# Kernel tuning notes

Measured on AMD Instinct MI355X. Metric: run time of the kernel, lower is better.

Reference implementation:

```python
import jax, jax.numpy as jnp
import numpy as np
from jax import lax

B, N, C = 32, 1024, 768
H_RES, W_RES = 32, 32
NUM_HEADS = 8
CH = C // NUM_HEADS  # 96
SCALE = CH ** -0.5


def setup_inputs() -> dict:
    key = jax.random.key(0)
    k1, k2, k3 = jax.random.split(key, 3)
    x = jax.random.normal(k1, (B, N, C), dtype=jnp.float32)
    # trunc_normal_(std=0.02) approximated by normal * 0.02
    w_qkv = jax.random.normal(k2, (3 * C, C), dtype=jnp.float32) * 0.02
    # conv init: normal(0, sqrt(2/fan_out)), fan_out = 3*3*C/groups = 9
    w_crpe = jax.random.normal(k3, (C, 1, 3, 3), dtype=jnp.float32) * np.sqrt(2.0 / 9.0)
    b_crpe = jnp.zeros((C,), dtype=jnp.float32)
    return {"x": x, "w_qkv": w_qkv, "w_crpe": w_crpe, "b_crpe": b_crpe}


def _forward(x, w_qkv, w_crpe, b_crpe):
    b, n, c = x.shape
    h, ch = NUM_HEADS, CH
    # qkv projection: [B,N,3C] -> [3,B,h,N,Ch]
    qkv = jnp.einsum('bnc,dc->bnd', x, w_qkv)
    qkv = qkv.reshape(b, n, 3, h, ch).transpose(2, 0, 3, 1, 4)
    q, k, v = qkv[0], qkv[1], qkv[2]  # each [B,h,N,Ch]
    # softmax over token dim (dim=2 of [B,h,N,Ch])
    k_softmax = jax.nn.softmax(k, axis=2)
    # dd_trans = k_softmax^T @ v : [B,h,Ch,Ch]
    dd_trans = jnp.einsum('bhnc,bhnd->bhcd', k_softmax, v)
    factor_attn = jnp.einsum('bhnc,bhcd->bhnd', q, dd_trans)  # [B,h,N,Ch]
    # crpe: depthwise 3x3 conv on v reshaped to image layout
    v_img = v.transpose(0, 1, 3, 2).reshape(b, c, H_RES, W_RES)  # B (h Ch) H W
    conv_v = lax.conv_general_dilated(
        v_img, w_crpe, window_strides=(1, 1), padding='SAME',
        feature_group_count=c,
        dimension_numbers=('NCHW', 'OIHW', 'NCHW'))
    conv_v = conv_v + b_crpe[None, :, None, None]
    conv_v = conv_v.reshape(b, h, ch, n).transpose(0, 1, 3, 2)  # [B,h,N,Ch]
    crpe = q * conv_v
    out = SCALE * factor_attn + crpe  # [B,h,N,Ch]
    return out.transpose(0, 2, 1, 3).reshape(b, n, c)


def reference(x, w_qkv, w_crpe, b_crpe):
    return _forward(x, w_qkv, w_crpe, b_crpe)
```

## Files before the change

kernel.cpp:

```cpp
#include <hip/hip_runtime.h>
#include <stdint.h>

#define B_SZ   32
#define N_TOK  1024
#define C_DIM  768
#define HEADS  8
#define CH_DIM 96
#define GM     32768
#define GN     2304
#define GK     768
#define SCALE_F 0.10206207261596577f
#define WHICH_STRIDE 25165824u
#define BH_STRIDE    98304u

typedef __attribute__((ext_vector_type(8))) short short8;
typedef __attribute__((ext_vector_type(8))) unsigned short ushort8;
typedef __attribute__((ext_vector_type(4))) float f32x4;
typedef __attribute__((ext_vector_type(4))) int int4v;

__device__ __forceinline__ float bf2f(unsigned short u) {
  union { unsigned int i; float f; } x; x.i = ((unsigned int)u) << 16; return x.f;
}
__device__ __forceinline__ unsigned short f2bf(float f) {
  union { float f; unsigned int i; } x; x.f = f;
  unsigned int r = x.i + 0x7fffu + ((x.i >> 16) & 1u);
  return (unsigned short)(r >> 16);
}

__device__ __forceinline__ void gload_lds16(const void* g, void* l) {
  __builtin_amdgcn_global_load_lds(
      (const __attribute__((address_space(1))) unsigned int*)g,
      (__attribute__((address_space(3))) unsigned int*)l, 16, 0, 0);
}

__global__ __launch_bounds__(256) void quant_rows(
    const float* __restrict__ x, const float* __restrict__ wq,
    signed char* __restrict__ xq, signed char* __restrict__ wqo,
    float* __restrict__ inv_x, float* __restrict__ inv_w) {
  const int row = blockIdx.x * 4 + (threadIdx.x >> 6);
  const int l = threadIdx.x & 63;
  const float* src; signed char* dst; float* inv; int r;
  if (row < GM) { src = x;  dst = xq;  inv = inv_x; r = row; }
  else { r = row - GM; if (r >= GN) return; src = wq; dst = wqo; inv = inv_w; }

  const float4* s4 = (const float4*)(src + (size_t)r * 768);
  float4 v0 = s4[l], v1 = s4[l + 64], v2 = s4[l + 128];
  float m = fmaxf(fmaxf(fmaxf(fabsf(v0.x), fabsf(v0.y)), fmaxf(fabsf(v0.z), fabsf(v0.w))),
                  fmaxf(fmaxf(fabsf(v1.x), fabsf(v1.y)), fmaxf(fabsf(v1.z), fabsf(v1.w))));
  m = fmaxf(m, fmaxf(fmaxf(fabsf(v2.x), fabsf(v2.y)), fmaxf(fabsf(v2.z), fabsf(v2.w))));
#pragma unroll
  for (int off = 32; off; off >>= 1) m = fmaxf(m, __shfl_xor(m, off));
  const float sc = 127.0f / m;
  if (l == 0) inv[r] = m * (1.0f / 127.0f);

  char4* d4 = (char4*)(dst + (size_t)r * 768);
  char4 o;
  o.x = (signed char)(int)rintf(v0.x * sc); o.y = (signed char)(int)rintf(v0.y * sc);
  o.z = (signed char)(int)rintf(v0.z * sc); o.w = (signed char)(int)rintf(v0.w * sc);
  d4[l] = o;
  o.x = (signed char)(int)rintf(v1.x * sc); o.y = (signed char)(int)rintf(v1.y * sc);
  o.z = (signed char)(int)rintf(v1.z * sc); o.w = (signed char)(int)rintf(v1.w * sc);
  d4[l + 64] = o;
  o.x = (signed char)(int)rintf(v2.x * sc); o.y = (signed char)(int)rintf(v2.y * sc);
  o.z = (signed char)(int)rintf(v2.z * sc); o.w = (signed char)(int)rintf(v2.w * sc);
  d4[l + 128] = o;
}

__global__ __launch_bounds__(512, 4) void qkv_gemm_i8(
    const signed char* __restrict__ xb,
    const signed char* __restrict__ wb,
    const float* __restrict__ inv_x,
    const float* __restrict__ inv_w,
    unsigned short* __restrict__ qkv) {
  __shared__ __align__(16) char lds[3][24576];

  const int t = threadIdx.x, w = t >> 6, l = t & 63;
  const int l15 = l & 15, lhi = l >> 4;

  const int bid = blockIdx.x;
  const int swz = (bid & 7) * 288 + (bid >> 3);
  const int brow = (swz / 9) * 128;
  const int bcol = (swz % 9) * 256;
  const int wr = w >> 2, wc = w & 3;

  const int s_colb = (((l & 3) ^ ((l >> 3) & 3)) << 4);
  const char* gA0 = (const char*)xb + (size_t)brow * 768 + s_colb;
  const char* gB0 = (const char*)wb + (size_t)bcol * 768 + s_colb;

  const int rd_sw = (lhi * 16) ^ (((l15 >> 1) & 3) << 4);
  const int a_off = (wr * 64 + l15) * 64 + rd_sw;
  const int b_off = 8192 + (wc * 64 + l15) * 64 + rd_sw;

  int4v acc[4][4];
#pragma unroll
  for (int m = 0; m < 4; ++m)
#pragma unroll
    for (int n = 0; n < 4; ++n) acc[m][n] = (int4v){0, 0, 0, 0};

  auto STAGE = [&](int bi, int kt) {
    const int rowL = w * 16 + (l >> 2);
    gload_lds16(gA0 + (size_t)rowL * 768 + kt * 64,         &lds[bi][w * 1024]);
    gload_lds16(gB0 + (size_t)rowL * 768 + kt * 64,         &lds[bi][8192 + w * 1024]);
    gload_lds16(gB0 + (size_t)(rowL + 128) * 768 + kt * 64, &lds[bi][8192 + (w + 8) * 1024]);
  };

  auto COMPUTE = [&](int bi) {
    int4v af[4], bf8[4];
#pragma unroll
    for (int n = 0; n < 4; ++n)
      bf8[n] = *(const int4v*)(&lds[bi][b_off + n * 1024]);
#pragma unroll
    for (int m = 0; m < 4; ++m)
      af[m] = *(const int4v*)(&lds[bi][a_off + m * 1024]);
    __builtin_amdgcn_s_setprio(1);
#pragma unroll
    for (int m = 0; m < 4; ++m)
#pragma unroll
      for (int n = 0; n < 4; ++n)
        acc[m][n] = __builtin_amdgcn_mfma_i32_16x16x64_i8(af[m], bf8[n], acc[m][n], 0, 0, 0);
    __builtin_amdgcn_s_setprio(0);
  };

#define SB __builtin_amdgcn_sched_barrier(0)
#define BAR do { SB; __builtin_amdgcn_s_barrier(); SB; } while (0)

  STAGE(0, 0); STAGE(1, 1); STAGE(2, 2);
  SB; asm volatile("s_waitcnt vmcnt(6)" ::: "memory");
  BAR;

#pragma unroll
  for (int kt = 0; kt < 12; ++kt) {
    COMPUTE(kt % 3);
    BAR;
    if (kt < 9) {
      STAGE(kt % 3, kt + 3);
      SB; asm volatile("s_waitcnt vmcnt(6)" ::: "memory");
    } else if (kt == 9) {
      SB; asm volatile("s_waitcnt vmcnt(3)" ::: "memory");
    } else if (kt == 10) {
      SB; asm volatile("s_waitcnt vmcnt(0)" ::: "memory");
    }
    BAR;
  }

  const int bb = brow / 1024;
#pragma unroll
  for (int m = 0; m < 4; ++m) {
    const int row0 = brow + wr * 64 + m * 16 + lhi * 4;
    const int tok0 = row0 & 1023;
    float ix[4];
#pragma unroll
    for (int r = 0; r < 4; ++r) ix[r] = inv_x[row0 + r];
#pragma unroll
    for (int n = 0; n < 4; ++n) {
      const int col   = bcol + wc * 64 + n * 16 + l15;
      const float dq0 = inv_w[col];
      const int which = col / 768;
      const int hh    = (col % 768) / 96;
      const int ch    = col % 96;
      unsigned short* dst = qkv + (size_t)which * WHICH_STRIDE
                          + ((size_t)(bb * 8 + hh)) * BH_STRIDE + ch;
#pragma unroll
      for (int r = 0; r < 4; ++r) {
        float v = (float)acc[m][n][r] * dq0 * ix[r];
        if (which == 1) v = __expf(v);
        dst[(size_t)(tok0 + r) * 96] = f2bf(v);
      }
    }
  }
#undef BAR
#undef SB
}

__global__ __launch_bounds__(512, 2) void dd_fused(
    const unsigned short* __restrict__ qkv,
    unsigned short* __restrict__ ddT) {
  __shared__ __align__(16) char smem[124416];
  unsigned short* stg = (unsigned short*)smem;
  float* facc = (float*)smem;
  float* fsum = (float*)(smem + 122880);
  float* sinv = (float*)(smem + 123648);

  const int bh = blockIdx.x;
  const int t = threadIdx.x, w = t >> 6, l = t & 63;
  const int l15 = l & 15, lhi = l >> 4;

  unsigned short* myK = stg + w * 7680;
  unsigned short* myV = myK + 3840;
  const int n   = l >> 1;
  const int chh = l & 1;
  const unsigned short* kb = qkv + WHICH_STRIDE     + (size_t)bh * BH_STRIDE;
  const unsigned short* vb = qkv + 2 * WHICH_STRIDE + (size_t)bh * BH_STRIDE;

  f32x4 acc[6][6], accS[6];
#pragma unroll
  for (int mf = 0; mf < 6; ++mf) {
    accS[mf] = (f32x4){0.f, 0.f, 0.f, 0.f};
#pragma unroll
    for (int nf = 0; nf < 6; ++nf) acc[mf][nf] = (f32x4){0.f, 0.f, 0.f, 0.f};
  }
  short8 ones;
#pragma unroll
  for (int j = 0; j < 8; ++j) ones[j] = (short)0x3F80;

  for (int tt = 0; tt < 4; ++tt) {
    const int n0 = w * 128 + tt * 32;
    const size_t g = (size_t)(n0 + n) * 96 + chh * 48;
#pragma unroll
    for (int i = 0; i < 6; ++i) {
      ushort8 k8 = *(const ushort8*)(kb + g + i * 8);
      ushort8 v8 = *(const ushort8*)(vb + g + i * 8);
      const int c0 = chh * 48 + i * 8;
#pragma unroll
      for (int j = 0; j < 8; ++j) {
        myK[(c0 + j) * 40 + n] = k8[j];
        myV[(c0 + j) * 40 + n] = v8[j];
      }
    }
    short8 af[6], bf8[6];
#pragma unroll
    for (int mf = 0; mf < 6; ++mf)
      af[mf] = *(const short8*)((const char*)myK + (mf * 16 + l15) * 80 + lhi * 16);
#pragma unroll
    for (int nf = 0; nf < 6; ++nf)
      bf8[nf] = *(const short8*)((const char*)myV + (nf * 16 + l15) * 80 + lhi * 16);
#pragma unroll
    for (int mf = 0; mf < 6; ++mf) {
#pragma unroll
      for (int nf = 0; nf < 6; ++nf)
        acc[mf][nf] = __builtin_amdgcn_mfma_f32_16x16x32_bf16(af[mf], bf8[nf], acc[mf][nf], 0, 0, 0);
      accS[mf] = __builtin_amdgcn_mfma_f32_16x16x32_bf16(af[mf], ones, accS[mf], 0, 0, 0);
    }
  }

  __syncthreads();
  float* fr  = facc + (w >> 2) * 9600;
  float* fsr = fsum + (w >> 2) * 96;
  for (int ww = 0; ww < 4; ++ww) {
    if ((w & 3) == ww) {
#pragma unroll
      for (int mf = 0; mf < 6; ++mf) {
#pragma unroll
        for (int nf = 0; nf < 6; ++nf) {
          const int c = mf * 16 + lhi * 4, d = nf * 16 + l15;
#pragma unroll
          for (int r = 0; r < 4; ++r) {
            float* p = fr + (size_t)(c + r) * 100 + d;
            if (ww == 0) *p = acc[mf][nf][r]; else *p += acc[mf][nf][r];
          }
        }
        if (l15 == 0) {
          const int c = mf * 16 + lhi * 4;
#pragma unroll
          for (int r = 0; r < 4; ++r) {
            if (ww == 0) fsr[c + r] = accS[mf][r];
            else         fsr[c + r] += accS[mf][r];
          }
        }
      }
    }
    __syncthreads();
  }
  for (int i = t; i < 9600; i += 512) facc[i] += facc[9600 + i];
  if (t < 96) fsum[t] += fsum[96 + t];
  __syncthreads();
  if (t < 96) sinv[t] = 1.0f / fsum[t];
  __syncthreads();

  unsigned short* dst = ddT + (size_t)bh * 9216;
#pragma unroll
  for (int e = 0; e < 18; ++e) {
    const int idx = t * 18 + e;
    const int d = idx / 96, c = idx % 96;
    dst[idx] = f2bf(facc[(size_t)c * 100 + d] * sinv[c]);
  }
}

__global__ __launch_bounds__(256, 2) void factor_conv_p(
    const unsigned short* __restrict__ qkv,
    const unsigned short* __restrict__ ddT,
    const float* __restrict__ wcr,
    const float* __restrict__ bcr,
    float* __restrict__ outb) {
  __shared__ __align__(16) unsigned short sQ[64 * 96];
  __shared__ __align__(16) unsigned short sD[96 * 96];
  __shared__ __align__(16) unsigned short sV[6 * 32 * 96];
  __shared__ float sW[96 * 9];
  __shared__ float sBias[96];
  const int half = blockIdx.x, h = blockIdx.y, b = blockIdx.z;
  const int t = threadIdx.x, wv = t >> 6, l = t & 63;
  const int l15 = l & 15, lhi = l >> 4;
  const int bh = b * 8 + h;

  const char* dg = (const char*)ddT + (size_t)bh * 18432;
#pragma unroll
  for (int it = 0; it < 4; ++it)
    gload_lds16(dg + (it * 256 + t) * 16, (char*)sD + it * 4096 + wv * 1024);
  if (wv < 2)
    gload_lds16(dg + (1024 + t) * 16, (char*)sD + 16384 + wv * 1024);
  for (int i = t; i < 960; i += 256) {
    if (i < 864) sW[i] = wcr[(size_t)(h * 96) * 9 + i];
    else         sBias[i - 864] = bcr[h * 96 + (i - 864)];
  }

  const char* qg = (const char*)(qkv + (size_t)bh * BH_STRIDE);
  const char* vg = (const char*)(qkv + 2 * WHICH_STRIDE + (size_t)bh * BH_STRIDE);
  const int wrow = (wv >> 1) * 32;
  const int wcol = (wv & 1) * 48;

  auto STAGE_ROW = [&](int y) {
    const int yy = y < 0 ? 0 : (y > 31 ? 31 : y);
    const int slot = (y + 1) % 6;
    const char* src = vg + (size_t)yy * 6144;
    char* dst = (char*)sV + slot * 6144;
    gload_lds16(src + t * 16, dst + wv * 1024);
    if (wv < 2)
      gload_lds16(src + 4096 + t * 16, dst + 4096 + wv * 1024);
  };

  const int Y0 = half * 16;
  STAGE_ROW(Y0 - 1); STAGE_ROW(Y0); STAGE_ROW(Y0 + 1); STAGE_ROW(Y0 + 2);

  for (int it8 = 0; it8 < 8; ++it8) {
    const int Y = Y0 + it8 * 2;
    const int n0 = Y * 32;

#pragma unroll
    for (int it = 0; it < 3; ++it)
      gload_lds16(qg + (size_t)n0 * 192 + (it * 256 + t) * 16,
                  (char*)sQ + it * 4096 + wv * 1024);
    if (it8 > 0) { STAGE_ROW(Y + 1); STAGE_ROW(Y + 2); }
    __syncthreads();

    f32x4 acc[2][3];
#pragma unroll
    for (int m = 0; m < 2; ++m)
#pragma unroll
      for (int nn = 0; nn < 3; ++nn) acc[m][nn] = (f32x4){0.f, 0.f, 0.f, 0.f};

#pragma unroll
    for (int ks = 0; ks < 3; ++ks) {
      short8 af[2], bf8[3];
#pragma unroll
      for (int m = 0; m < 2; ++m)
        af[m] = *(const short8*)((const char*)sQ + (wrow + m*16 + l15) * 192 + ks * 64 + lhi * 16);
#pragma unroll
      for (int nn = 0; nn < 3; ++nn)
        bf8[nn] = *(const short8*)((const char*)sD + (wcol + nn*16 + l15) * 192 + ks * 64 + lhi * 16);
#pragma unroll
      for (int m = 0; m < 2; ++m)
#pragma unroll
        for (int nn = 0; nn < 3; ++nn)
          acc[m][nn] = __builtin_amdgcn_mfma_f32_16x16x32_bf16(af[m], bf8[nn], acc[m][nn], 0, 0, 0);
    }

#pragma unroll
    for (int nn = 0; nn < 3; ++nn) {
      const int dc = wcol + nn * 16 + l15;
      float w9[9];
#pragma unroll
      for (int k = 0; k < 9; ++k) w9[k] = sW[dc * 9 + k];
      const float bv = sBias[dc];
#pragma unroll
      for (int m = 0; m < 2; ++m) {
        const int rl0 = wrow + m * 16 + lhi * 4;
        const int x = rl0 & 31, yl = rl0 >> 5;
        float cs[3][6];
#pragma unroll
        for (int dy = 0; dy < 3; ++dy) {
          const int gy = Y + yl + dy - 1;
          const bool vy = (gy >= 0) && (gy < 32);
          const int slot = (gy + 1) % 6;
#pragma unroll
          for (int i = 0; i < 6; ++i) {
            const int xx = x - 1 + i;
            cs[dy][i] = (vy && xx >= 0 && xx < 32)
                ? bf2f(sV[slot * 3072 + xx * 96 + dc]) : 0.f;
          }
        }
#pragma unroll
        for (int r = 0; r < 4; ++r) {
          float conv = bv;
#pragma unroll
          for (int dy = 0; dy < 3; ++dy)
#pragma unroll
            for (int dx = 0; dx < 3; ++dx)
              conv += w9[dy * 3 + dx] * cs[dy][r + dx];
          const int row = rl0 + r;
          const float qv = bf2f(sQ[row * 96 + dc]);
          outb[((size_t)(b * N_TOK + n0 + row)) * C_DIM + h * 96 + dc] =
              SCALE_F * acc[m][nn][r] + qv * conv;
        }
      }
    }
    __syncthreads();
  }
}

extern "C" void kernel_launch(void* const* d_in, const int* in_sizes, int n_in,
                              void* d_out, int out_size, void* d_ws, size_t ws_size,
                              hipStream_t stream) {
  const float* x      = (const float*)d_in[0];
  const float* w_qkv  = (const float*)d_in[1];
  const float* w_crpe = (const float*)d_in[2];
  const float* b_crpe = (const float*)d_in[3];
  float* out = (float*)d_out;

  char* ws = (char*)d_ws;
  signed char*    xq    = (signed char*)ws;
  signed char*    wq    = (signed char*)(ws + 25165824);
  float*          inv_x = (float*)(ws + 27000832);
  float*          inv_w = (float*)(ws + 27131904);
  unsigned short* qkv   = (unsigned short*)(ws + 53870592);
  unsigned short* ddT   = (unsigned short*)(ws + 204865536);

  quant_rows<<<dim3((GM + GN + 3) / 4), 256, 0, stream>>>(
      x, w_qkv, xq, wq, inv_x, inv_w);
  qkv_gemm_i8<<<dim3(2304), 512, 0, stream>>>(xq, wq, inv_x, inv_w, qkv);
  dd_fused<<<dim3(B_SZ * HEADS), 512, 0, stream>>>(qkv, ddT);
  factor_conv_p<<<dim3(2, HEADS, B_SZ), 256, 0, stream>>>(qkv, ddT, w_crpe, b_crpe, out);
}
```

Measured before the change: 208.0 us.

## Make int8 QKV GEMM persistent with cross-tile prefetch pipeline

The int8 QKV GEMM now launches 512 persistent workgroups, each looping over 4 or 5 output tiles instead of one workgroup per tile. The triple-buffered LDS pipeline carries across tile boundaries, so loads for the next tile's first K-steps are issued while the current tile finishes and its epilogue runs. This removes per-block launch/prologue cost and pipeline drain bubbles. The trade-offs are a tail imbalance (256 blocks do one extra tile), some redundant dummy loads at the very end, and a K loop that is no longer unrolled.

```diff
diff --git a/kernel.cpp b/kernel.cpp
--- a/kernel.cpp
+++ b/kernel.cpp
@@ -76,32 +76,33 @@
 
   const int t = threadIdx.x, w = t >> 6, l = t & 63;
   const int l15 = l & 15, lhi = l >> 4;
-
   const int bid = blockIdx.x;
-  const int swz = (bid & 7) * 288 + (bid >> 3);
-  const int brow = (swz / 9) * 128;
-  const int bcol = (swz % 9) * 256;
+  const int ntile = 4 + (bid < 256);
   const int wr = w >> 2, wc = w & 3;
 
   const int s_colb = (((l & 3) ^ ((l >> 3) & 3)) << 4);
-  const char* gA0 = (const char*)xb + (size_t)brow * 768 + s_colb;
-  const char* gB0 = (const char*)wb + (size_t)bcol * 768 + s_colb;
+  const int rowL = w * 16 + (l >> 2);
 
   const int rd_sw = (lhi * 16) ^ (((l15 >> 1) & 3) << 4);
   const int a_off = (wr * 64 + l15) * 64 + rd_sw;
   const int b_off = 8192 + (wc * 64 + l15) * 64 + rd_sw;
 
   int4v acc[4][4];
-#pragma unroll
-  for (int m = 0; m < 4; ++m)
-#pragma unroll
-    for (int n = 0; n < 4; ++n) acc[m][n] = (int4v){0, 0, 0, 0};
-
-  auto STAGE = [&](int bi, int kt) {
-    const int rowL = w * 16 + (l >> 2);
-    gload_lds16(gA0 + (size_t)rowL * 768 + kt * 64,         &lds[bi][w * 1024]);
-    gload_lds16(gB0 + (size_t)rowL * 768 + kt * 64,         &lds[bi][8192 + w * 1024]);
-    gload_lds16(gB0 + (size_t)(rowL + 128) * 768 + kt * 64, &lds[bi][8192 + (w + 8) * 1024]);
+
+  auto TILE_RC = [&](int ti, int& br, int& bc) {
+    const int swz = (ti & 7) * 288 + (ti >> 3);
+    br = (swz / 9) * 128;
+    bc = (swz % 9) * 256;
+  };
+
+  auto STAGE = [&](int bi, int si, int sk) {
+    int gti = bid + si * 512;
+    int br, bc; TILE_RC(gti, br, bc);
+    const char* gA = (const char*)xb + (size_t)br * 768 + s_colb;
+    const char* gB = (const char*)wb + (size_t)bc * 768 + s_colb;
+    gload_lds16(gA + (size_t)rowL * 768 + sk * 64,         &lds[bi][w * 1024]);
+    gload_lds16(gB + (size_t)rowL * 768 + sk * 64,         &lds[bi][8192 + w * 1024]);
+    gload_lds16(gB + (size_t)(rowL + 128) * 768 + sk * 64, &lds[bi][8192 + (w + 8) * 1024]);
   };
 
   auto COMPUTE = [&](int bi) {
@@ -124,47 +125,53 @@
 #define SB __builtin_amdgcn_sched_barrier(0)
 #define BAR do { SB; __builtin_amdgcn_s_barrier(); SB; } while (0)
 
-  STAGE(0, 0); STAGE(1, 1); STAGE(2, 2);
+  STAGE(0, 0, 0); STAGE(1, 0, 1); STAGE(2, 0, 2);
   SB; asm volatile("s_waitcnt vmcnt(6)" ::: "memory");
   BAR;
 
-#pragma unroll
-  for (int kt = 0; kt < 12; ++kt) {
-    COMPUTE(kt % 3);
-    BAR;
-    if (kt < 9) {
-      STAGE(kt % 3, kt + 3);
+  for (int i = 0; i < ntile; ++i) {
+    const int ti = bid + i * 512;
+    int brow, bcol; TILE_RC(ti, brow, bcol);
+
+#pragma unroll
+    for (int m = 0; m < 4; ++m)
+#pragma unroll
+      for (int n = 0; n < 4; ++n) acc[m][n] = (int4v){0, 0, 0, 0};
+
+    for (int kt = 0; kt < 12; ++kt) {
+      COMPUTE(kt % 3);
+      BAR;
+      int si = i, sk = kt + 3;
+      if (sk >= 12) { si = i + 1; sk -= 12; }
+      if (si >= ntile) { si = 0; sk = 0; }
+      STAGE(kt % 3, si, sk);
       SB; asm volatile("s_waitcnt vmcnt(6)" ::: "memory");
-    } else if (kt == 9) {
-      SB; asm volatile("s_waitcnt vmcnt(3)" ::: "memory");
-    } else if (kt == 10) {
-      SB; asm volatile("s_waitcnt vmcnt(0)" ::: "memory");
-    }
-    BAR;
-  }
-
-  const int bb = brow / 1024;
-#pragma unroll
-  for (int m = 0; m < 4; ++m) {
-    const int row0 = brow + wr * 64 + m * 16 + lhi * 4;
-    const int tok0 = row0 & 1023;
-    float ix[4];
-#pragma unroll
-    for (int r = 0; r < 4; ++r) ix[r] = inv_x[row0 + r];
-#pragma unroll
-    for (int n = 0; n < 4; ++n) {
-      const int col   = bcol + wc * 64 + n * 16 + l15;
-      const float dq0 = inv_w[col];
-      const int which = col / 768;
-      const int hh    = (col % 768) / 96;
-      const int ch    = col % 96;
-      unsigned short* dst = qkv + (size_t)which * WHICH_STRIDE
-                          + ((size_t)(bb * 8 + hh)) * BH_STRIDE + ch;
-#pragma unroll
-      for (int r = 0; r < 4; ++r) {
-        float v = (float)acc[m][n][r] * dq0 * ix[r];
-        if (which == 1) v = __expf(v);
-        dst[(size_t)(tok0 + r) * 96] = f2bf(v);
+      BAR;
+    }
+
+    const int bb = brow / 1024;
+#pragma unroll
+    for (int m = 0; m < 4; ++m) {
+      const int row0 = brow + wr * 64 + m * 16 + lhi * 4;
+      const int tok0 = row0 & 1023;
+      float ix[4];
+#pragma unroll
+      for (int r = 0; r < 4; ++r) ix[r] = inv_x[row0 + r];
+#pragma unroll
+      for (int n = 0; n < 4; ++n) {
+        const int col   = bcol + wc * 64 + n * 16 + l15;
+        const float dq0 = inv_w[col];
+        const int which = col / 768;
+        const int hh    = (col % 768) / 96;
+        const int ch    = col % 96;
+        unsigned short* dst = qkv + (size_t)which * WHICH_STRIDE
+                            + ((size_t)(bb * 8 + hh)) * BH_STRIDE + ch;
+#pragma unroll
+        for (int r = 0; r < 4; ++r) {
+          float v = (float)acc[m][n][r] * dq0 * ix[r];
+          if (which == 1) v = __expf(v);
+          dst[(size_t)(tok0 + r) * 96] = f2bf(v);
+        }
       }
     }
   }
@@ -416,7 +423,7 @@
 
   quant_rows<<<dim3((GM + GN + 3) / 4), 256, 0, stream>>>(
       x, w_qkv, xq, wq, inv_x, inv_w);
-  qkv_gemm_i8<<<dim3(2304), 512, 0, stream>>>(xq, wq, inv_x, inv_w, qkv);
+  qkv_gemm_i8<<<dim3(512), 512, 0, stream>>>(xq, wq, inv_x, inv_w, qkv);
   dd_fused<<<dim3(B_SZ * HEADS), 512, 0, stream>>>(qkv, ddT);
   factor_conv_p<<<dim3(2, HEADS, B_SZ), 256, 0, stream>>>(qkv, ddT, w_crpe, b_crpe, out);
 }
```

Result: slower. 213.8 us (+2.8%).
